# Kernel optimization log

Measured on AMD Instinct MI355X. Metric: run time of the kernel, lower is better.

Reference implementation:

```python
import jax, jax.numpy as jnp
import numpy as np

DEPTH = 10
LEAF = 2 ** DEPTH          # 1024 leaves
NODE_NUM = 2 * LEAF - 1    # 2047
N = NODE_NUM + 1           # 2048 nodes incl. global node 0
ATTN = 4
D = 128
B = 8
L = 2


def _trace_children(ni):
    terms = []
    s, e = ni << 1, (ni << 1) | 1
    while s <= NODE_NUM and e <= NODE_NUM:
        terms.extend(range(s, e + 1))
        s <<= 1
        e = (e << 1) | 1
    return terms


def _trace_left(si):
    ni, cd, terms, stop = si + LEAF, DEPTH, [], False
    while not stop:
        cs = ni - ATTN + 1 - ((ni - ATTN + 1) & 1)
        stop = cs < 2 ** cd
        cs = max(2 ** cd, cs)
        terms.extend(range(cs, ni + 1))
        ni = (cs - 1) >> 1
        cd -= 1
    return terms


def _trace_right(ei):
    ni, cd, terms, stop = ei + LEAF, DEPTH, [], False
    while not stop:
        ce = ni + ATTN - 1 + ((ni - ATTN) & 1)
        stop = ce >= 2 ** (cd + 1)
        ce = min(2 ** (cd + 1) - 1, ce)
        terms.extend(range(ni, ce + 1))
        ni = (ce + 1) >> 1
        cd -= 1
    return terms


def _build_edges():
    src, dst = [], []
    for ni in range(1, NODE_NUM + 1):
        if ni < LEAF:
            t = _trace_children(ni)
        else:
            t = _trace_left(ni - LEAF) + _trace_right(ni - LEAF)
        src.extend(t)
        dst.extend([ni] * len(t))
    e = np.stack([np.asarray(src, np.int64), np.asarray(dst, np.int64)])  # [2, E]
    off = np.arange(B, dtype=np.int64) * N
    eb = (e[:, None, :] + off[None, :, None]).reshape(2, -1)  # batch-offset like _fetch_edge_data
    return eb.astype(np.int32)


def setup_inputs() -> dict:
    key = jax.random.key(0)
    k0, k1, k2 = jax.random.split(key, 3)
    s = 1.0 / np.sqrt(D)
    return {
        "elements": jax.random.normal(k0, (B, LEAF, D), jnp.float32),
        "ln_gamma": jnp.ones((L, D), jnp.float32),
        "ln_beta": jnp.zeros((L, D), jnp.float32),
        "w_nei": (jax.random.normal(k1, (L, D, D), jnp.float32) * s),
        "b_nei": jnp.zeros((L, D), jnp.float32),
        "w_root": (jax.random.normal(k2, (L, D, D), jnp.float32) * s),
        "edge_index": jnp.asarray(_build_edges()),
    }


def _sinusoid(pos, d):
    # ArbitraryPositionEncoder: sinusoidal encoding over (possibly negative) positions
    half = d // 2
    inv = jnp.exp(-jnp.arange(half, dtype=jnp.float32) * (np.log(10000.0) / half))
    ang = pos[:, None] * inv[None, :]  # [n, half]
    return jnp.stack([jnp.sin(ang), jnp.cos(ang)], -1).reshape(pos.shape[0], d)


def reference(elements, ln_gamma, ln_beta, w_nei, b_nei, w_root, edge_index):
    Bx, leaf, d = elements.shape
    depth = int(np.log2(leaf))
    # bottom-up tree compression (mean of two children)
    cur = elements
    levels = [cur]
    for _ in range(depth):
        cur = 0.5 * (cur[:, 0::2] + cur[:, 1::2])
        levels.append(cur)
    # node ordering: [global node 0 (=-1), root (level 0), ..., leaves (level depth)]
    node_feat = jnp.concatenate(
        [jnp.full((Bx, 1, d), -1.0, elements.dtype)] + levels[::-1], axis=1)  # [B, N, D]
    n = node_feat.shape[1]
    # positional encoding: vertical = floor(log2(idx)), horizontal = idx - 2^vertical
    idx = jnp.arange(n, dtype=jnp.float32)
    vpos = jnp.floor(jnp.log2(jnp.where(idx == 0, 0.5, idx)))
    hpos = idx - jnp.exp2(vpos)
    enc = jnp.concatenate([_sinusoid(hpos, d // 2), _sinusoid(vpos, d // 2)], -1)  # [N, D]
    x = (node_feat + enc[None]).reshape(Bx * n, d)
    src, dst = edge_index[0], edge_index[1]
    nseg = Bx * n
    deg = jnp.maximum(
        jax.ops.segment_sum(jnp.ones(src.shape, jnp.float32), dst, num_segments=nseg), 1.0)
    # DeepGCNLayer res+ blocks with SAGEConv (mean aggr)
    for l in range(ln_gamma.shape[0]):
        mu = jnp.mean(x, -1, keepdims=True)
        var = jnp.mean((x - mu) ** 2, -1, keepdims=True)
        h = (x - mu) * jax.lax.rsqrt(var + 1e-5) * ln_gamma[l] + ln_beta[l]
        h = jax.nn.gelu(h, approximate=False)
        agg = jax.ops.segment_sum(h[src], dst, num_segments=nseg) / deg[:, None]
        h = agg @ w_nei[l] + b_nei[l] + h @ w_root[l]
        x = x + h
    return x.reshape(Bx, n, d)
```

## Files before the change

### kernel.cpp

```cpp
#include <hip/hip_runtime.h>
#include <hip/hip_bf16.h>

#define LEAFN 1024
#define NN    2048
#define BATCH 8
#define DD    128
#define ROWS  (BATCH*NN)
#define AHS   384
#define NB    256
#define NT    1024

#define LOG1E4_OVER_32 0.28782313662425575f

#define SLACK 9
#define CSTRIDE 136
#define SB_OFF   0
#define SBT      520
#define MSK_OFF  58240
#define DEG_OFF  59264
#define FB_OFF   59392
#define AGGL_OFF 0
#define RED_OFF  61440
#define RED2_OFF 62464

typedef __bf16 bf16x8 __attribute__((ext_vector_type(8)));
typedef float  floatx4 __attribute__((ext_vector_type(4)));
typedef float  floatx2 __attribute__((ext_vector_type(2)));

__device__ __forceinline__ float bf2f(unsigned short u) {
  return __uint_as_float(((unsigned)u) << 16);
}
__device__ __forceinline__ unsigned short f2bf(float f) {
  unsigned u = __float_as_uint(f);
  u += 0x7FFFu + ((u >> 16) & 1u);
  return (unsigned short)(u >> 16);
}
__device__ __forceinline__ float gelu(float v) {
  return 0.5f * v * (1.0f + erff(v * 0.70710678118f));
}
__device__ __forceinline__ floatx2 bfpair(unsigned u) {
  floatx2 r;
  r[0] = __uint_as_float(u << 16);
  r[1] = __uint_as_float(u & 0xffff0000u);
  return r;
}

__device__ __forceinline__ float enc_val(int node, int d) {
  float hp, vp;
  if (node == 0) { hp = -0.5f; vp = -1.0f; }
  else {
    int v = 31 - __clz(node);
    hp = (float)(node - (1 << v));
    vp = (float)v;
  }
  float pos = (d < 64) ? hp : vp;
  int i = ((d < 64) ? d : (d - 64)) >> 1;
  float inv = __expf(-(float)i * LOG1E4_OVER_32);
  float ang = pos * inv;
  return (d & 1) ? __cosf(ang) : __sinf(ang);
}

__device__ __forceinline__ void win_cd(int jb, int cd, int& lo_, int& wd_) {
  int g0 = 1024 + jb * 32, g1 = g0 + 31;
  int a0 = g0 >> (10 - cd), a1 = g1 >> (10 - cd);
  int l = a0 - SLACK, h = a1 + SLACK;
  int lvlo = 1 << cd, lvhi = (2 << cd) - 1;
  lo_ = l < lvlo ? lvlo : l;
  int hh = h > lvhi ? lvhi : h;
  int w = hh - lo_ + 1;
  wd_ = w < 0 ? 0 : w;
}

__device__ __forceinline__ void gbarN(int* bar, int slot) {
  __syncthreads();
  if (threadIdx.x == 0) {
    int g = blockIdx.x & 7;
    int* base = bar + (slot * 8 + g) * 64;
    __threadfence();
    if (__hip_atomic_fetch_add(base, 1, __ATOMIC_RELAXED,
                               __HIP_MEMORY_SCOPE_AGENT) == 31)
      __hip_atomic_store(base + 32, 1, __ATOMIC_RELAXED,
                         __HIP_MEMORY_SCOPE_AGENT);
    while (!__hip_atomic_load(base + 32, __ATOMIC_RELAXED,
                              __HIP_MEMORY_SCOPE_AGENT))
      __builtin_amdgcn_s_sleep(1);
    __threadfence();
  }
  __syncthreads();
}

__device__ __forceinline__ void st_agg(unsigned short* ah, int b, int g, int j,
                                       floatx4 S, float inv) {
  ushort4 o;
  o.x = f2bf(S[0] * inv); o.y = f2bf(S[1] * inv);
  o.z = f2bf(S[2] * inv); o.w = f2bf(S[3] * inv);
  *(ushort4*)&ah[(size_t)(b * NN + g) * AHS + j * 4] = o;
}

__device__ __forceinline__ void ph_tree(char* smemc, int b, int s,
                                        const float* __restrict__ elements,
                                        float* __restrict__ x,
                                        float* __restrict__ lvl4,
                                        unsigned short* __restrict__ ah,
                                        const float* __restrict__ gamma,
                                        const float* __restrict__ beta,
                                        float* __restrict__ sroot,
                                        float* xci, int* bar) {
  float* sm = (float*)smemc;
  floatx4* smv = (floatx4*)smemc;
  int tid = threadIdx.x;
  const float4* src = (const float4*)(elements + (size_t)(b * LEAFN + s * 64) * DD);
  for (int i = tid; i < 2048; i += NT) {
    int f = i * 4;
    int j = f >> 7, d = f & 127;
    *(float4*)&sm[(63 + j) * DD + d] = src[i];
  }
  __syncthreads();
  {
    for (int idx = tid; idx < 16 * 32; idx += NT) {
      int k = 16 + (idx >> 5), j = idx & 31;
      floatx4 a = 0.5f * (smv[(4 * k - 1) * 32 + j] + smv[(4 * k) * 32 + j]);
      floatx4 c = 0.5f * (smv[(4 * k + 1) * 32 + j] + smv[(4 * k + 2) * 32 + j]);
      smv[(2 * k - 1) * 32 + j] = a;
      smv[(2 * k) * 32 + j] = c;
      smv[(k - 1) * 32 + j] = 0.5f * (a + c);
    }
    __syncthreads();
    for (int idx = tid; idx < 4 * 32; idx += NT) {
      int k = 4 + (idx >> 5), j = idx & 31;
      floatx4 a = 0.5f * (smv[(4 * k - 1) * 32 + j] + smv[(4 * k) * 32 + j]);
      floatx4 c = 0.5f * (smv[(4 * k + 1) * 32 + j] + smv[(4 * k + 2) * 32 + j]);
      smv[(2 * k - 1) * 32 + j] = a;
      smv[(2 * k) * 32 + j] = c;
      smv[(k - 1) * 32 + j] = 0.5f * (a + c);
    }
    __syncthreads();
    for (int idx = tid; idx < 32; idx += NT) {
      int j = idx;
      floatx4 a = 0.5f * (smv[3 * 32 + j] + smv[4 * 32 + j]);
      floatx4 c = 0.5f * (smv[5 * 32 + j] + smv[6 * 32 + j]);
      smv[1 * 32 + j] = a;
      smv[2 * 32 + j] = c;
      floatx4 r = 0.5f * (a + c);
      smv[j] = r;
      ((floatx4*)&lvl4[(size_t)(b * 16 + s) * DD])[j] = r;
    }
  }
  __syncthreads();
  if (tid == 0) {
    __threadfence();
    __hip_atomic_store(bar + 1536 + b * 64 + s * 4, 1, __ATOMIC_RELAXED,
                       __HIP_MEMORY_SCOPE_AGENT);
  }
  {
    int d2 = tid & 63;
    int i = d2 & 31;
    float inv = __expf(-(float)i * LOG1E4_OVER_32);
    bool lowhalf = d2 < 32;
    for (int idx2 = tid; idx2 < 127 * 64; idx2 += NT) {
      int row = idx2 >> 6;
      int k = row + 1;
      int lv = 31 - __clz(k);
      int g = ((16 + s) << lv) | (k - (1 << lv));
      float vp = (float)(lv + 4);
      float hp = (float)(g - (16 << lv));
      float pos = lowhalf ? hp : vp;
      float sv, cv;
      __sincosf(pos * inv, &sv, &cv);
      int base = row * DD + 2 * d2;
      float xv0 = sm[base] + sv;
      float xv1 = sm[base + 1] + cv;
      sm[base] = xv0; sm[base + 1] = xv1;
      if (k >= 64 || k <= 32) {
        float2 o = make_float2(xv0, xv1);
        *(float2*)&x[((size_t)(b * NN + g)) * DD + 2 * d2] = o;
      }
    }
  }
  __syncthreads();
// ... 61 lines not shown
      floatx4 sk = (smv[(2 * k - 1) * 32 + j] + smv[(2 * k) * 32 + j]) + (sa + sc);
      smv[(4 * k - 1) * 32 + j] = sa;
      smv[(4 * k + 1) * 32 + j] = sc;
      smv[(2 * k - 1) * 32 + j] = sk;
      st_agg(ah, b, ((16 + s) << 5) | (2 * k - 32), j, sa, 0.5f);
      st_agg(ah, b, ((16 + s) << 5) | (2 * k + 1 - 32), j, sc, 0.5f);
      st_agg(ah, b, ((16 + s) << 4) | (k - 16), j, sk, 1.0f / 6.0f);
    }
    __syncthreads();
    for (int idx = tid; idx < 4 * 32; idx += NT) {
      int k = 4 + (idx >> 5), j = idx & 31;
      floatx4 sa = (smv[(4 * k - 1) * 32 + j] + smv[(4 * k) * 32 + j]) +
                   (smv[(8 * k - 1) * 32 + j] + smv[(8 * k + 1) * 32 + j]);
      floatx4 sc = (smv[(4 * k + 1) * 32 + j] + smv[(4 * k + 2) * 32 + j]) +
                   (smv[(8 * k + 3) * 32 + j] + smv[(8 * k + 5) * 32 + j]);
      floatx4 sk = (smv[(2 * k - 1) * 32 + j] + smv[(2 * k) * 32 + j]) + (sa + sc);
      smv[(4 * k - 1) * 32 + j] = sa;
      smv[(4 * k + 1) * 32 + j] = sc;
      smv[(2 * k - 1) * 32 + j] = sk;
      st_agg(ah, b, ((16 + s) << 3) | (2 * k - 8), j, sa, 1.0f / 14.0f);
      st_agg(ah, b, ((16 + s) << 3) | (2 * k + 1 - 8), j, sc, 1.0f / 14.0f);
      st_agg(ah, b, ((16 + s) << 2) | (k - 4), j, sk, 1.0f / 30.0f);
    }
    __syncthreads();
    for (int idx = tid; idx < 32; idx += NT) {
      int j = idx;
      floatx4 sa = (smv[3 * 32 + j] + smv[4 * 32 + j]) +
                   (smv[7 * 32 + j] + smv[9 * 32 + j]);
      floatx4 sc = (smv[5 * 32 + j] + smv[6 * 32 + j]) +
                   (smv[11 * 32 + j] + smv[13 * 32 + j]);
      floatx4 sk = (smv[1 * 32 + j] + smv[2 * 32 + j]) + (sa + sc);
      st_agg(ah, b, ((16 + s) << 1) | 0, j, sa, 1.0f / 62.0f);
      st_agg(ah, b, ((16 + s) << 1) | 1, j, sc, 1.0f / 62.0f);
      st_agg(ah, b, (16 + s), j, sk, 1.0f / 126.0f);
      ((floatx4*)&sroot[(size_t)(b * 16 + s) * DD])[j] = sk;
    }
  }
}

__device__ __forceinline__ void ph_top(char* smemc, int b,
                                       const float* __restrict__ lvl4,
                                       unsigned short* __restrict__ ah,
                                       const float* __restrict__ gamma,
                                       const float* __restrict__ beta) {
  float (*xs)[DD] = (float(*)[DD])smemc;
  int tid = threadIdx.x;
  if (tid < 128) {
    int d = tid;
    float v[16];
    for (int j = 0; j < 16; ++j) v[j] = lvl4[(b * 16 + j) * DD + d];
    for (int j = 0; j < 8; ++j) v[j] = 0.5f * (v[2 * j] + v[2 * j + 1]);
    for (int j = 0; j < 8; ++j) xs[8 + j][d] = v[j] + enc_val(8 + j, d);
    for (int j = 0; j < 4; ++j) v[j] = 0.5f * (v[2 * j] + v[2 * j + 1]);
    for (int j = 0; j < 4; ++j) xs[4 + j][d] = v[j] + enc_val(4 + j, d);
    for (int j = 0; j < 2; ++j) v[j] = 0.5f * (v[2 * j] + v[2 * j + 1]);
    for (int j = 0; j < 2; ++j) xs[2 + j][d] = v[j] + enc_val(2 + j, d);
    v[0] = 0.5f * (v[0] + v[1]);
    xs[1][d] = v[0] + enc_val(1, d);
    xs[0][d] = -1.0f + enc_val(0, d);
  }
  __syncthreads();
  if (tid < 128) {
    int rr = tid >> 3, sub = tid & 7, dp = sub * 16;
    float w[16], s1 = 0.f, s2 = 0.f;
#pragma unroll
    for (int j = 0; j < 16; ++j) { w[j] = xs[rr][dp + j]; s1 += w[j]; s2 += w[j] * w[j]; }
    s1 += __shfl_xor(s1, 1); s2 += __shfl_xor(s2, 1);
    s1 += __shfl_xor(s1, 2); s2 += __shfl_xor(s2, 2);
    s1 += __shfl_xor(s1, 4); s2 += __shfl_xor(s2, 4);
    float mu = s1 * (1.0f / 128.0f);
    float var = s2 * (1.0f / 128.0f) - mu * mu;
    float rinv = rsqrtf(var + 1e-5f);
    __attribute__((aligned(16))) unsigned short o[16];
#pragma unroll
    for (int j = 0; j < 16; ++j)
      o[j] = f2bf(gelu((w[j] - mu) * rinv * gamma[dp + j] + beta[dp + j]));
    unsigned short* dst = &ah[(size_t)(b * NN + rr) * AHS + 128 + dp];
    *(uint4*)&dst[0] = *(uint4*)&o[0];
    *(uint4*)&dst[8] = *(uint4*)&o[8];
  }
  __syncthreads();
}

__device__ __forceinline__ void ph_aggsub(char* smemc, int b, int s,
                                          unsigned short* ah,
                                          float* __restrict__ sroot) {
  floatx4 (*S)[32] = (floatx4(*)[32])smemc;
  int tid = threadIdx.x;
  for (int idx = tid; idx < 32 * 32; idx += NT) {
    int k = 32 + (idx >> 5), q = idx & 31;
    int c = (16 + s) * 64 + (2 * k - 64);
    size_t a0 = (size_t)(b * NN + c) * AHS + 256 + q * 4;
    ushort4 u0 = *(const ushort4*)&ah[a0];
    ushort4 u1 = *(const ushort4*)&ah[a0 + AHS];
    floatx4 v;
    v[0] = bf2f(u0.x) + bf2f(u1.x);
    v[1] = bf2f(u0.y) + bf2f(u1.y);
    v[2] = bf2f(u0.z) + bf2f(u1.z);
    v[3] = bf2f(u0.w) + bf2f(u1.w);
    S[k][q] = v;
    st_agg(ah, b, (16 + s) * 32 + (k - 32), q, v, 0.5f);
  }
  __syncthreads();
  for (int idx = tid; idx < 8 * 32; idx += NT) {
    int k = 8 + (idx >> 5), q = idx & 31;
    size_t aa = (size_t)(b * NN + (((16 + s) << 5) | (4 * k - 32))) * AHS + 256 + q * 4;
    ushort4 u0 = *(const ushort4*)&ah[aa];
    ushort4 u1 = *(const ushort4*)&ah[aa + AHS];
    size_t ab = (size_t)(b * NN + (((16 + s) << 5) | (4 * k + 2 - 32))) * AHS + 256 + q * 4;
    ushort4 w0 = *(const ushort4*)&ah[ab];
    ushort4 w1 = *(const ushort4*)&ah[ab + AHS];
    size_t ac = (size_t)(b * NN + (((16 + s) << 4) | (2 * k - 16))) * AHS + 256 + q * 4;
    ushort4 h0 = *(const ushort4*)&ah[ac];
    ushort4 h1 = *(const ushort4*)&ah[ac + AHS];
    floatx4 s4a, s4b, s3;
    floatx4 sc0 = S[4 * k][q], sc1 = S[4 * k + 1][q];
    floatx4 sd0 = S[4 * k + 2][q], sd1 = S[4 * k + 3][q];
    s4a[0] = bf2f(u0.x) + bf2f(u1.x) + sc0[0] + sc1[0];
    s4a[1] = bf2f(u0.y) + bf2f(u1.y) + sc0[1] + sc1[1];
    s4a[2] = bf2f(u0.z) + bf2f(u1.z) + sc0[2] + sc1[2];
    s4a[3] = bf2f(u0.w) + bf2f(u1.w) + sc0[3] + sc1[3];
    s4b[0] = bf2f(w0.x) + bf2f(w1.x) + sd0[0] + sd1[0];
    s4b[1] = bf2f(w0.y) + bf2f(w1.y) + sd0[1] + sd1[1];
    s4b[2] = bf2f(w0.z) + bf2f(w1.z) + sd0[2] + sd1[2];
    s4b[3] = bf2f(w0.w) + bf2f(w1.w) + sd0[3] + sd1[3];
    s3[0] = bf2f(h0.x) + bf2f(h1.x) + s4a[0] + s4b[0];
    s3[1] = bf2f(h0.y) + bf2f(h1.y) + s4a[1] + s4b[1];
    s3[2] = bf2f(h0.z) + bf2f(h1.z) + s4a[2] + s4b[2];
    s3[3] = bf2f(h0.w) + bf2f(h1.w) + s4a[3] + s4b[3];
    S[2 * k][q] = s4a; S[2 * k + 1][q] = s4b; S[k][q] = s3;
    st_agg(ah, b, ((16 + s) << 4) | (2 * k - 16), q, s4a, 1.0f / 6.0f);
    st_agg(ah, b, ((16 + s) << 4) | (2 * k + 1 - 16), q, s4b, 1.0f / 6.0f);
    st_agg(ah, b, ((16 + s) << 3) | (k - 8), q, s3, 1.0f / 14.0f);
  }
  __syncthreads();
  for (int idx = tid; idx < 2 * 32; idx += NT) {
    int k = 2 + (idx >> 5), q = idx & 31;
    size_t aa = (size_t)(b * NN + (((16 + s) << 3) | (4 * k - 8))) * AHS + 256 + q * 4;
    ushort4 u0 = *(const ushort4*)&ah[aa];
    ushort4 u1 = *(const ushort4*)&ah[aa + AHS];
    size_t ab = (size_t)(b * NN + (((16 + s) << 3) | (4 * k + 2 - 8))) * AHS + 256 + q * 4;
    ushort4 w0 = *(const ushort4*)&ah[ab];
    ushort4 w1 = *(const ushort4*)&ah[ab + AHS];
    size_t ac = (size_t)(b * NN + (((16 + s) << 2) | (2 * k - 4))) * AHS + 256 + q * 4;
    ushort4 h0 = *(const ushort4*)&ah[ac];
    ushort4 h1 = *(const ushort4*)&ah[ac + AHS];
    floatx4 s2a, s2b, s1v;
    floatx4 sc0 = S[4 * k][q], sc1 = S[4 * k + 1][q];
    floatx4 sd0 = S[4 * k + 2][q], sd1 = S[4 * k + 3][q];
    s2a[0] = bf2f(u0.x) + bf2f(u1.x) + sc0[0] + sc1[0];
    s2a[1] = bf2f(u0.y) + bf2f(u1.y) + sc0[1] + sc1[1];
    s2a[2] = bf2f(u0.z) + bf2f(u1.z) + sc0[2] + sc1[2];
    s2a[3] = bf2f(u0.w) + bf2f(u1.w) + sc0[3] + sc1[3];
    s2b[0] = bf2f(w0.x) + bf2f(w1.x) + sd0[0] + sd1[0];
    s2b[1] = bf2f(w0.y) + bf2f(w1.y) + sd0[1] + sd1[1];
    s2b[2] = bf2f(w0.z) + bf2f(w1.z) + sd0[2] + sd1[2];
    s2b[3] = bf2f(w0.w) + bf2f(w1.w) + sd0[3] + sd1[3];
    s1v[0] = bf2f(h0.x) + bf2f(h1.x) + s2a[0] + s2b[0];
    s1v[1] = bf2f(h0.y) + bf2f(h1.y) + s2a[1] + s2b[1];
    s1v[2] = bf2f(h0.z) + bf2f(h1.z) + s2a[2] + s2b[2];
    s1v[3] = bf2f(h0.w) + bf2f(h1.w) + s2a[3] + s2b[3];
    S[2 * k][q] = s2a; S[2 * k + 1][q] = s2b; S[k][q] = s1v;
    st_agg(ah, b, ((16 + s) << 2) | (2 * k - 4), q, s2a, 1.0f / 30.0f);
    st_agg(ah, b, ((16 + s) << 2) | (2 * k + 1 - 4), q, s2b, 1.0f / 30.0f);
    st_agg(ah, b, ((16 + s) << 1) | (k - 2), q, s1v, 1.0f / 62.0f);
  }
  __syncthreads();
  for (int idx = tid; idx < 32; idx += NT) {
    int q = idx;
    size_t aa = (size_t)(b * NN + (((16 + s) << 1) | 0)) * AHS + 256 + q * 4;
    ushort4 u0 = *(const ushort4*)&ah[aa];
    ushort4 u1 = *(const ushort4*)&ah[aa + AHS];
    floatx4 sc0 = S[2][q], sc1 = S[3][q];
    floatx4 s0v;
    s0v[0] = bf2f(u0.x) + bf2f(u1.x) + sc0[0] + sc1[0];
    s0v[1] = bf2f(u0.y) + bf2f(u1.y) + sc0[1] + sc1[1];
    s0v[2] = bf2f(u0.z) + bf2f(u1.z) + sc0[2] + sc1[2];
    s0v[3] = bf2f(u0.w) + bf2f(u1.w) + sc0[3] + sc1[3];
    st_agg(ah, b, (16 + s), q, s0v, 1.0f / 126.0f);
    ((floatx4*)sroot)[(size_t)(b * 16 + s) * 32 + q] = s0v;
  }
}

__device__ __forceinline__ void ph_leafagg(char* smemc, int b, int jb,
                                           const int* __restrict__ srcv,
                                           const int* __restrict__ dstv,
                                           const int* __restrict__ s0a,
                                           const int* __restrict__ s1a,
                                           const unsigned short* __restrict__ eoff,
                                           unsigned short* ah, int hoff,
                                           int build) {
  int tid = threadIdx.x;
  int lane = tid & 63, wv = tid >> 6;
  unsigned short* SB = (unsigned short*)(smemc + SB_OFF);
  unsigned* msk = (unsigned*)(smemc + MSK_OFF);
  float* invdeg = (float*)(smemc + DEG_OFF);
  unsigned int* fb = (unsigned int*)(smemc + FB_OFF);
  unsigned short* aggl = (unsigned short*)(smemc + AGGL_OFF);
  int rbase = b * NN + 1024 + jb * 32;

  int lo[11], wd[11], off[11];
  int acc_off = 0;
#pragma unroll
  for (int cd = 10; cd >= 1; --cd) {
    win_cd(jb, cd, lo[cd], wd[cd]);
    off[cd] = acc_off;
    acc_off += wd[cd];
  }

  for (int t = tid; t < 3640; t += NT)
    ((uint4*)smemc)[t] = make_uint4(0, 0, 0, 0);
  if (build) {
    if (tid < 256) msk[tid] = 0u;
    if (tid >= 256 && tid < 288)
      invdeg[tid - 256] = 1.0f /
          (float)max(s1a[rbase + tid - 256] - s0a[rbase + tid - 256], 1);
    if (tid == 288) *fb = 0u;
  }
  __syncthreads();

  if (build) {
    int E0 = s0a[rbase], E1 = s1a[rbase + 31];
    for (int e = E0 + tid; e < E1; e += NT) {
      int leaf = dstv[e] - rbase;
      unsigned kr = eoff[e];
      if (kr == 0xFFFFu) atomicOr(fb, 1u << leaf);
      else atomicOr(&msk[leaf * 8 + (kr >> 5)], 1u << (kr & 31));
    }
  }
#pragma unroll
  for (int cd = 10; cd >= 1; --cd) {
    int w = wd[cd];
    for (int t = tid; t < w * 16; t += NT) {
      int row = t >> 4, seg = t & 15;
      int kr = off[cd] + row;
      uint4 u = *(const uint4*)&ah[(size_t)(b * NN + lo[cd] + row) * AHS + hoff + seg * 8];
      unsigned short* p = SB + ((kr >> 5) * 8 + (seg >> 1)) * SBT +
                          ((kr & 31) >> 3) * 128 + (seg & 1) * 64 + (kr & 7);
      p[0]  = (unsigned short)(u.x & 0xffff);
      p[8]  = (unsigned short)(u.x >> 16);
      p[16] = (unsigned short)(u.y & 0xffff);
      p[24] = (unsigned short)(u.y >> 16);
      p[32] = (unsigned short)(u.z & 0xffff);
      p[40] = (unsigned short)(u.z >> 16);
      p[48] = (unsigned short)(u.w & 0xffff);
      p[56] = (unsigned short)(u.w >> 16);
    }
  }
  __syncthreads();

  int m = lane & 15, q = lane >> 4;
  int mt = wv >> 3, nt = wv & 7;
  int arow = mt * 16 + m;
  floatx4 acc = (floatx4){0.f, 0.f, 0.f, 0.f};
#pragma unroll
  for (int kcl = 0; kcl < 7; ++kcl) {
    unsigned mw = msk[arow * 8 + kcl];
    unsigned bits = (mw >> (q * 8)) & 0xffu;
    union { uint4 u; bf16x8 v; } A;
    A.u.x = ((bits & 1u)  ? 0x3F80u : 0u) | ((bits & 2u)   ? 0x3F800000u : 0u);
    A.u.y = ((bits & 4u)  ? 0x3F80u : 0u) | ((bits & 8u)   ? 0x3F800000u : 0u);
    A.u.z = ((bits & 16u) ? 0x3F80u : 0u) | ((bits & 32u)  ? 0x3F800000u : 0u);
    A.u.w = ((bits & 64u) ? 0x3F80u : 0u) | ((bits & 128u) ? 0x3F800000u : 0u);
    bf16x8 bb = *(const bf16x8*)&SB[(kcl * 8 + nt) * SBT + lane * 8];
    acc = __builtin_amdgcn_mfma_f32_16x16x32_bf16(A.v, bb, acc, 0, 0, 0);
  }
  __syncthreads();

  unsigned fbm = *fb;
#pragma unroll
  for (int r = 0; r < 4; ++r) {
    int leaf = mt * 16 + q * 4 + r;
    if (!((fbm >> leaf) & 1u))
      aggl[leaf * CSTRIDE + nt * 16 + m] = f2bf(acc[r] * invdeg[leaf]);
  }
  if (fbm && tid < 512) {
    int leaf = tid >> 4, c = tid & 15;
    if ((fbm >> leaf) & 1u) {
      int e0 = s0a[rbase + leaf], e1 = s1a[rbase + leaf];
      floatx2 a0 = {0.f, 0.f}, a1 = {0.f, 0.f}, a2 = {0.f, 0.f}, a3 = {0.f, 0.f};
      for (int e = e0; e < e1; ++e) {
        int g = srcv[e] - b * NN;
        uint4 u = *(const uint4*)&ah[(size_t)(b * NN + g) * AHS + hoff + c * 8];
        a0 += bfpair(u.x); a1 += bfpair(u.y); a2 += bfpair(u.z); a3 += bfpair(u.w);
      }
      float inv = 1.0f / (float)max(e1 - e0, 1);
      __attribute__((aligned(16))) unsigned short o[8];
      o[0] = f2bf(a0[0] * inv); o[1] = f2bf(a0[1] * inv);
      o[2] = f2bf(a1[0] * inv); o[3] = f2bf(a1[1] * inv);
      o[4] = f2bf(a2[0] * inv); o[5] = f2bf(a2[1] * inv);
      o[6] = f2bf(a3[0] * inv); o[7] = f2bf(a3[1] * inv);
      *(uint4*)&aggl[leaf * CSTRIDE + c * 8] = *(uint4*)&o[0];
    }
  }
}

__device__ __forceinline__ void ph_topfin(int b,
                                          const float* __restrict__ sroot,
                                          unsigned short* ah, int hoff) {
  int d = threadIdx.x;
  float S16[16], h16[16], Sv[16];
#pragma unroll
  for (int j = 0; j < 16; ++j) S16[j] = sroot[(size_t)(b * 16 + j) * DD + d];
#pragma unroll
  for (int j = 0; j < 16; ++j)
    h16[j] = bf2f(ah[(size_t)(b * NN + 16 + j) * AHS + hoff + d]);
#pragma unroll
  for (int k = 8; k < 16; ++k)
    Sv[k] = h16[2 * k - 16] + h16[2 * k - 15] + S16[2 * k - 16] + S16[2 * k - 15];
#pragma unroll
  for (int k = 7; k >= 1; --k)
    Sv[k] = bf2f(ah[(size_t)(b * NN + 2 * k) * AHS + hoff + d]) +
            bf2f(ah[(size_t)(b * NN + 2 * k + 1) * AHS + hoff + d]) +
            Sv[2 * k] + Sv[2 * k + 1];
#pragma unroll
  for (int k = 1; k < 16; ++k) {
    int dv = 31 - __clz(k);
    float inv = 1.0f / (float)((1 << (11 - dv)) - 2);
    ah[(size_t)(b * NN + k) * AHS + d] = f2bf(Sv[k] * inv);
  }
  ah[(size_t)(b * NN) * AHS + d] = f2bf(0.0f);
}

__device__ __forceinline__ void ph_gemm32(char* redc, const unsigned short* aggl,
                                          int rowbase, unsigned short* ah,
                                          const unsigned short* __restrict__ wfl,
                                          const float* __restrict__ bn,
                                          float* __restrict__ x, int hoff_in,
                                          const float* __restrict__ gamma,
                                          const float* __restrict__ beta,
                                          float* xc, int first_layer) {
  int wave = threadIdx.x >> 6, lane = threadIdx.x & 63;
  bool act = wave < 8;
  int wl = wave & 7;
  int mt = wl >> 2, nq = wl & 3;
  int r0 = rowbase + mt * 16;
  int m = lane & 15, q = lane >> 4;
  floatx4 acc[2];
  acc[0] = (floatx4){0.f, 0.f, 0.f, 0.f};
  acc[1] = (floatx4){0.f, 0.f, 0.f, 0.f};
  if (act) {
    const unsigned short* arow = ah + (size_t)(r0 + m) * AHS + q * 8;
    const bf16x8* B = (const bf16x8*)wfl + lane;
#pragma unroll
    for (int kc = 0; kc < 8; ++kc) {
      bf16x8 a0;
      if (kc < 4)
        a0 = *(const bf16x8*)&aggl[(mt * 16 + m) * CSTRIDE + kc * 32 + q * 8];
      else
        a0 = *(const bf16x8*)(arow + hoff_in + (kc - 4) * 32);
#pragma unroll
      for (int ci = 0; ci < 2; ++ci) {
        bf16x8 bb = B[(kc * 8 + nq * 2 + ci) * 64];
        acc[ci] = __builtin_amdgcn_mfma_f32_16x16x32_bf16(a0, bb, acc[ci], 0, 0, 0);
      }
    }
  }
  if (first_layer) {
    float s1[4] = {0.f, 0.f, 0.f, 0.f}, s2[4] = {0.f, 0.f, 0.f, 0.f};
    if (act) {
#pragma unroll
      for (int ci = 0; ci < 2; ++ci) {
        int col = (nq * 2 + ci) * 16 + m;
        float bias = bn[col];
#pragma unroll
        for (int r = 0; r < 4; ++r) {
          int row = r0 + q * 4 + r;
          float v = x[(size_t)row * DD + col] + acc[ci][r] + bias;
          xc[ci * 4 + r] = v;
          s1[r] += v; s2[r] += v * v;
        }
      }
#pragma unroll
      for (int r = 0; r < 4; ++r) {
        s1[r] += __shfl_xor(s1[r], 1); s2[r] += __shfl_xor(s2[r], 1);
// ... 181 lines not shown
  floatx4 acc = (floatx4){0.f, 0.f, 0.f, 0.f};
  int col = (ct & 7) * 16 + m;
  if (act) {
    const unsigned short* arow = ah + (size_t)(b * NN + m) * AHS + q * 8;
    const bf16x8* B = (const bf16x8*)wfl + lane;
#pragma unroll
    for (int kc = 0; kc < 8; ++kc) {
      int koff = (kc < 4) ? kc * 32 : hoff_in + (kc - 4) * 32;
      bf16x8 a0 = *(const bf16x8*)(arow + koff);
      bf16x8 bb = B[(kc * 8 + ct) * 64];
      acc = __builtin_amdgcn_mfma_f32_16x16x32_bf16(a0, bb, acc, 0, 0, 0);
    }
  }
  if (first_layer) {
    float s1[4] = {0.f, 0.f, 0.f, 0.f}, s2[4] = {0.f, 0.f, 0.f, 0.f};
    float bias = act ? bn[col] : 0.f;
    if (act) {
#pragma unroll
      for (int r = 0; r < 4; ++r) {
        float v = xc[r] + acc[r] + bias;
        xc[r] = v; s1[r] = v; s2[r] = v * v;
      }
#pragma unroll
      for (int r = 0; r < 4; ++r) {
        s1[r] += __shfl_xor(s1[r], 1); s2[r] += __shfl_xor(s2[r], 1);
        s1[r] += __shfl_xor(s1[r], 2); s2[r] += __shfl_xor(s2[r], 2);
        s1[r] += __shfl_xor(s1[r], 4); s2[r] += __shfl_xor(s2[r], 4);
        s1[r] += __shfl_xor(s1[r], 8); s2[r] += __shfl_xor(s2[r], 8);
      }
    }
    float* red = (float*)redc;
    __syncthreads();
    if (act && m == 0) {
#pragma unroll
      for (int r = 0; r < 4; ++r) {
        red[(q * 4 + r) * 8 + ct] = s1[r];
        red[128 + (q * 4 + r) * 8 + ct] = s2[r];
      }
    }
    __syncthreads();
    if (act) {
#pragma unroll
      for (int r = 0; r < 4; ++r) {
        float t1 = 0.f, t2 = 0.f;
#pragma unroll
        for (int j = 0; j < 8; ++j) {
          t1 += red[(q * 4 + r) * 8 + j];
          t2 += red[128 + (q * 4 + r) * 8 + j];
        }
        float mu = t1 * (1.0f / 128.0f);
        float var = t2 * (1.0f / 128.0f) - mu * mu;
        float rv = rsqrtf(var + 1e-5f);
        float hh = gelu((xc[r] - mu) * rv * gamma[col] + beta[col]);
        ah[(size_t)(b * NN + q * 4 + r) * AHS + 256 + col] = f2bf(hh);
      }
    }
  } else {
    if (act) {
      float bias = bn[col];
#pragma unroll
      for (int r = 0; r < 4; ++r)
        x[(size_t)(b * NN + q * 4 + r) * DD + col] = xc[r] + acc[r] + bias;
    }
  }
}

__global__ __launch_bounds__(NT, 1) void k_mega(
    const float* __restrict__ elements, const float* __restrict__ ln_gamma,
    const float* __restrict__ ln_beta, const float* __restrict__ w_nei,
    const float* __restrict__ b_nei, const float* __restrict__ w_root,
    const int* __restrict__ srcv, const int* __restrict__ dstv, int E,
    float* __restrict__ x, int* s0a, int* s1a, float* lvl4, float* sroot,
    unsigned short* wf, unsigned short* ah, unsigned short* eoff, int* bar) {
  __shared__ __align__(16) char smem[65536];
  int bid = blockIdx.x, tid = threadIdx.x;
  int b = bid & 7, gb = bid >> 3;
  int Eb = E >> 3;
  unsigned short* wfg = wf + (size_t)b * 65536;
  float xcl[8], xci[8], xct[4];
  int wv = tid >> 6;

  if (gb < 16) {
    ph_tree(smem, b, gb, elements, x, lvl4, ah, ln_gamma, ln_beta, sroot, xci, bar);
  } else if (gb < 24) {
    int base = b * Eb;
    for (int i = base + (gb - 16) * NT + tid; i < base + Eb; i += 8 * NT) {
      int dv = dstv[i];
      if (i == 0 || dstv[i - 1] != dv) s0a[dv] = i;
      if (i == base + Eb - 1 || dstv[i + 1] != dv) s1a[dv] = i + 1;
    }
    for (int i = base + (gb - 16) * NT + tid; i < base + Eb; i += 8 * NT) {
      int dl = dstv[i] - b * NN - 1024;
      unsigned short ov = 0xFFFFu;
      if (dl >= 0) {
        int jb2 = dl >> 5;
        int g = srcv[i] - b * NN;
        int lv = 31 - __clz(g);
        int acc2 = 0;
#pragma unroll
        for (int cd = 10; cd >= 1; --cd) {
          int lo_, wd_;
          win_cd(jb2, cd, lo_, wd_);
          if (cd == lv) {
            int idx = g - lo_;
            if ((unsigned)idx < (unsigned)wd_)
              ov = (unsigned short)(acc2 + idx);
          }
          acc2 += wd_;
        }
      }
      eoff[i] = ov;
    }
  } else if (gb < 28) {
    int gi = (gb - 24) * NT + tid;
    int lane = gi & 63, ct = (gi >> 6) & 7, kc = gi >> 9;
    int n = ct * 16 + (lane & 15);
    int k = kc * 32 + (lane >> 4) * 8;
    int kk = k & 127;
#pragma unroll
    for (int l = 0; l < 2; ++l) {
      const float* w = (k < 128) ? (w_nei + (size_t)l * DD * DD)
                                 : (w_root + (size_t)l * DD * DD);
      unsigned short* o = wfg + (size_t)l * 32768 + (size_t)gi * 8;
#pragma unroll
      for (int j = 0; j < 8; ++j) o[j] = f2bf(w[(size_t)(kk + j) * DD + n]);
    }
  } else if (gb == 28) {
    if (tid < 16) {
      while (!__hip_atomic_load(bar + 1536 + b * 64 + tid * 4, __ATOMIC_RELAXED,
                                __HIP_MEMORY_SCOPE_AGENT))
        __builtin_amdgcn_s_sleep(1);
      __threadfence();
    }
    __syncthreads();
    ph_top(smem, b, lvl4, ah, ln_gamma, ln_beta);
    {
      int ln = tid & 63, m_ = ln & 15, q_ = ln >> 4;
      if (wv < 8) {
        float (*xs)[DD] = (float(*)[DD])smem;
#pragma unroll
        for (int r = 0; r < 4; ++r) xct[r] = xs[q_ * 4 + r][wv * 16 + m_];
      }
    }
  }
  gbarN(bar, 0);

  if (gb == 28) {
    if (tid < 128) ph_topfin(b, sroot, ah, 128);
    __syncthreads();
    ph_gemm16t(smem + RED_OFF, b, ah, wfg, b_nei, x, 128,
               ln_gamma + DD, ln_beta + DD, xct, 1);
    __syncthreads();
  }
  ph_leafagg(smem, b, gb, srcv, dstv, s0a, s1a, eoff, ah, 128, 1);
  __syncthreads();
  if (wv < 8) {
    ph_gemm32(smem + RED_OFF, (const unsigned short*)(smem + AGGL_OFF),
              b * NN + 1024 + gb * 32, ah, wfg, b_nei, x, 128,
              ln_gamma + DD, ln_beta + DD, xcl, 1);
  } else if (gb < 16) {
    ph_gemm32s(smem + RED2_OFF, b, gb, 32, ah, wfg, b_nei, x, 128,
               ln_gamma + DD, ln_beta + DD, xci, 1, nullptr);
  } else {
    ph_gemm32s(smem + RED2_OFF, b, gb - 16, 0, ah, wfg, b_nei, x, 128,
               ln_gamma + DD, ln_beta + DD, xci, 1, x);
  }
  gbarN(bar, 1);

  if (gb < 16) {
    ph_aggsub(smem, b, gb, ah, sroot);
    __syncthreads();
    if (tid == 0) {
      __threadfence();
      __hip_atomic_store(bar + 1024 + b * 64 + gb * 4, 1, __ATOMIC_RELAXED,
                         __HIP_MEMORY_SCOPE_AGENT);
    }
  }
  ph_leafagg(smem, b, gb, srcv, dstv, s0a, s1a, eoff, ah, 256, 0);
  if (gb >= 16 && tid == 0) {
    while (!__hip_atomic_load(bar + 1024 + b * 64 + (gb - 16) * 4, __ATOMIC_RELAXED,
                              __HIP_MEMORY_SCOPE_AGENT))
      __builtin_amdgcn_s_sleep(1);
    __threadfence();
  }
  __syncthreads();
  if (wv < 8) {
    ph_gemm32(smem + RED_OFF, (const unsigned short*)(smem + AGGL_OFF),
              b * NN + 1024 + gb * 32, ah, wfg + 32768, b_nei + DD,
              x, 256, ln_gamma, ln_beta, xcl, 0);
  } else if (gb < 16) {
    ph_gemm32s(smem + RED2_OFF, b, gb, 32, ah, wfg + 32768, b_nei + DD, x, 256,
               ln_gamma, ln_beta, xci, 0, nullptr);
  } else {
    ph_gemm32s(smem + RED2_OFF, b, gb - 16, 0, ah, wfg + 32768, b_nei + DD, x, 256,
               ln_gamma, ln_beta, xci, 0, nullptr);
  }
  if (gb == 28) {
    if (tid < 16) {
      while (!__hip_atomic_load(bar + 1024 + b * 64 + tid * 4, __ATOMIC_RELAXED,
                                __HIP_MEMORY_SCOPE_AGENT))
        __builtin_amdgcn_s_sleep(1);
      __threadfence();
    }
    __syncthreads();
    if (tid < 128) ph_topfin(b, sroot, ah, 256);
    __syncthreads();
    ph_gemm16t(smem + RED_OFF, b, ah, wfg + 32768, b_nei + DD, x, 256,
               ln_gamma, ln_beta, xct, 0);
  }
}

extern "C" void kernel_launch(void* const* d_in, const int* in_sizes, int n_in,
                              void* d_out, int out_size, void* d_ws, size_t ws_size,
                              hipStream_t stream) {
  const float* elements = (const float*)d_in[0];
  const float* ln_gamma = (const float*)d_in[1];
  const float* ln_beta  = (const float*)d_in[2];
  const float* w_nei    = (const float*)d_in[3];
  const float* b_nei    = (const float*)d_in[4];
  const float* w_root   = (const float*)d_in[5];
  const int*   edge     = (const int*)d_in[6];
  int E = in_sizes[6] / 2;
  const int* srcv = edge;
  const int* dstv = edge + E;
  float* x = (float*)d_out;

  char* ws = (char*)d_ws;
  int*            bar   = (int*)ws;
  int*            s0    = (int*)(ws + 65536);
  int*            s1    = (int*)(ws + 131072);
  float*          lvl4  = (float*)(ws + 196608);
  float*          sroot = (float*)(ws + 262144);
  unsigned short* wf    = (unsigned short*)(ws + 327680);
  unsigned short* ah    = (unsigned short*)(ws + 327680 + 1048576);
  unsigned short* eoff  = (unsigned short*)(ws + 327680 + 1048576 + 12582912);

  hipMemsetAsync(bar, 0, 8192, stream);
  k_mega<<<dim3(NB), dim3(NT), 0, stream>>>(
      elements, ln_gamma, ln_beta, w_nei, b_nei, w_root,
      srcv, dstv, E, x, s0, s1, lvl4, sroot, wf, ah, eoff, bar);
}
```

Baseline: 158.1 us.

## Overlap subtree aggregation with leaf aggregation using warp specialization

Folds the separate subtree aggregation phase into the leaf aggregation routine. Waves 14-15 (threads 896+) run the per-column subtree sums from registers while the other waves stage the neighbour tile and run the MFMA mask-matmul. The MFMA now uses 8 waves, each doing two 16-row tiles. The shared-memory zeroing is narrowed to the tail rows, and the mask clearing is moved before the global barrier. This removes several block-wide syncs and serial phases, but puts a 64-float register array on the specialist threads, which may raise register pressure.

```diff
diff --git a/kernel.cpp b/kernel.cpp
--- a/kernel.cpp
+++ b/kernel.cpp
@@ -95,6 +95,65 @@
   o.x = f2bf(S[0] * inv); o.y = f2bf(S[1] * inv);
   o.z = f2bf(S[2] * inv); o.w = f2bf(S[3] * inv);
   *(ushort4*)&ah[(size_t)(b * NN + g) * AHS + j * 4] = o;
+}
+
+__device__ __forceinline__ void aggsub_A(int b, int s, unsigned short* ah,
+                                         float* S, int d) {
+#pragma unroll
+  for (int k = 32; k < 64; ++k) {
+    int c = ((16 + s) << 6) | (2 * k - 64);
+    size_t a = (size_t)(b * NN + c) * AHS + 256 + d;
+    float v = bf2f(ah[a]) + bf2f(ah[a + AHS]);
+    S[k] = v;
+    ah[(size_t)(b * NN + (((16 + s) << 5) | (k - 32))) * AHS + d] = f2bf(v * 0.5f);
+  }
+#pragma unroll
+  for (int k = 16; k < 32; ++k) {
+    int c = ((16 + s) << 5) | (2 * k - 32);
+    size_t a = (size_t)(b * NN + c) * AHS + 256 + d;
+    float v = bf2f(ah[a]) + bf2f(ah[a + AHS]) + S[2 * k] + S[2 * k + 1];
+    S[k] = v;
+    ah[(size_t)(b * NN + (((16 + s) << 4) | (k - 16))) * AHS + d] =
+        f2bf(v * (1.0f / 6.0f));
+  }
+}
+__device__ __forceinline__ void aggsub_B(int b, int s, unsigned short* ah,
+                                         float* __restrict__ sroot,
+                                         float* S, int d) {
+#pragma unroll
+  for (int k = 8; k < 16; ++k) {
+    int c = ((16 + s) << 4) | (2 * k - 16);
+    size_t a = (size_t)(b * NN + c) * AHS + 256 + d;
+    float v = bf2f(ah[a]) + bf2f(ah[a + AHS]) + S[2 * k] + S[2 * k + 1];
+    S[k] = v;
+    ah[(size_t)(b * NN + (((16 + s) << 3) | (k - 8))) * AHS + d] =
+        f2bf(v * (1.0f / 14.0f));
+  }
+#pragma unroll
+  for (int k = 4; k < 8; ++k) {
+    int c = ((16 + s) << 3) | (2 * k - 8);
+    size_t a = (size_t)(b * NN + c) * AHS + 256 + d;
+    float v = bf2f(ah[a]) + bf2f(ah[a + AHS]) + S[2 * k] + S[2 * k + 1];
+    S[k] = v;
+    ah[(size_t)(b * NN + (((16 + s) << 2) | (k - 4))) * AHS + d] =
+        f2bf(v * (1.0f / 30.0f));
+  }
+#pragma unroll
+  for (int k = 2; k < 4; ++k) {
+    int c = ((16 + s) << 2) | (2 * k - 4);
+    size_t a = (size_t)(b * NN + c) * AHS + 256 + d;
+    float v = bf2f(ah[a]) + bf2f(ah[a + AHS]) + S[2 * k] + S[2 * k + 1];
+    S[k] = v;
+    ah[(size_t)(b * NN + (((16 + s) << 1) | (k - 2))) * AHS + d] =
+        f2bf(v * (1.0f / 62.0f));
+  }
+  {
+    int c = (16 + s) << 1;
+    size_t a = (size_t)(b * NN + c) * AHS + 256 + d;
+    float v = bf2f(ah[a]) + bf2f(ah[a + AHS]) + S[2] + S[3];
+    ah[(size_t)(b * NN + (16 + s)) * AHS + d] = f2bf(v * (1.0f / 126.0f));
+    sroot[(size_t)(b * 16 + s) * DD + d] = v;
+  }
 }
 
 __device__ __forceinline__ void ph_tree(char* smemc, int b, int s,
@@ -322,106 +381,6 @@
   __syncthreads();
 }
 
-__device__ __forceinline__ void ph_aggsub(char* smemc, int b, int s,
-                                          unsigned short* ah,
-                                          float* __restrict__ sroot) {
-  floatx4 (*S)[32] = (floatx4(*)[32])smemc;
-  int tid = threadIdx.x;
-  for (int idx = tid; idx < 32 * 32; idx += NT) {
-    int k = 32 + (idx >> 5), q = idx & 31;
-    int c = (16 + s) * 64 + (2 * k - 64);
-    size_t a0 = (size_t)(b * NN + c) * AHS + 256 + q * 4;
-    ushort4 u0 = *(const ushort4*)&ah[a0];
-    ushort4 u1 = *(const ushort4*)&ah[a0 + AHS];
-    floatx4 v;
-    v[0] = bf2f(u0.x) + bf2f(u1.x);
-    v[1] = bf2f(u0.y) + bf2f(u1.y);
-    v[2] = bf2f(u0.z) + bf2f(u1.z);
-    v[3] = bf2f(u0.w) + bf2f(u1.w);
-    S[k][q] = v;
-    st_agg(ah, b, (16 + s) * 32 + (k - 32), q, v, 0.5f);
-  }
-  __syncthreads();
-  for (int idx = tid; idx < 8 * 32; idx += NT) {
-    int k = 8 + (idx >> 5), q = idx & 31;
-    size_t aa = (size_t)(b * NN + (((16 + s) << 5) | (4 * k - 32))) * AHS + 256 + q * 4;
-    ushort4 u0 = *(const ushort4*)&ah[aa];
-    ushort4 u1 = *(const ushort4*)&ah[aa + AHS];
-    size_t ab = (size_t)(b * NN + (((16 + s) << 5) | (4 * k + 2 - 32))) * AHS + 256 + q * 4;
-    ushort4 w0 = *(const ushort4*)&ah[ab];
-    ushort4 w1 = *(const ushort4*)&ah[ab + AHS];
-    size_t ac = (size_t)(b * NN + (((16 + s) << 4) | (2 * k - 16))) * AHS + 256 + q * 4;
-    ushort4 h0 = *(const ushort4*)&ah[ac];
-    ushort4 h1 = *(const ushort4*)&ah[ac + AHS];
-    floatx4 s4a, s4b, s3;
-    floatx4 sc0 = S[4 * k][q], sc1 = S[4 * k + 1][q];
-    floatx4 sd0 = S[4 * k + 2][q], sd1 = S[4 * k + 3][q];
-    s4a[0] = bf2f(u0.x) + bf2f(u1.x) + sc0[0] + sc1[0];
-    s4a[1] = bf2f(u0.y) + bf2f(u1.y) + sc0[1] + sc1[1];
-    s4a[2] = bf2f(u0.z) + bf2f(u1.z) + sc0[2] + sc1[2];
-    s4a[3] = bf2f(u0.w) + bf2f(u1.w) + sc0[3] + sc1[3];
-    s4b[0] = bf2f(w0.x) + bf2f(w1.x) + sd0[0] + sd1[0];
-    s4b[1] = bf2f(w0.y) + bf2f(w1.y) + sd0[1] + sd1[1];
-    s4b[2] = bf2f(w0.z) + bf2f(w1.z) + sd0[2] + sd1[2];
-    s4b[3] = bf2f(w0.w) + bf2f(w1.w) + sd0[3] + sd1[3];
-    s3[0] = bf2f(h0.x) + bf2f(h1.x) + s4a[0] + s4b[0];
-    s3[1] = bf2f(h0.y) + bf2f(h1.y) + s4a[1] + s4b[1];
-    s3[2] = bf2f(h0.z) + bf2f(h1.z) + s4a[2] + s4b[2];
-    s3[3] = bf2f(h0.w) + bf2f(h1.w) + s4a[3] + s4b[3];
-    S[2 * k][q] = s4a; S[2 * k + 1][q] = s4b; S[k][q] = s3;
-    st_agg(ah, b, ((16 + s) << 4) | (2 * k - 16), q, s4a, 1.0f / 6.0f);
-    st_agg(ah, b, ((16 + s) << 4) | (2 * k + 1 - 16), q, s4b, 1.0f / 6.0f);
-    st_agg(ah, b, ((16 + s) << 3) | (k - 8), q, s3, 1.0f / 14.0f);
-  }
-  __syncthreads();
-  for (int idx = tid; idx < 2 * 32; idx += NT) {
-    int k = 2 + (idx >> 5), q = idx & 31;
-    size_t aa = (size_t)(b * NN + (((16 + s) << 3) | (4 * k - 8))) * AHS + 256 + q * 4;
-    ushort4 u0 = *(const ushort4*)&ah[aa];
-    ushort4 u1 = *(const ushort4*)&ah[aa + AHS];
-    size_t ab = (size_t)(b * NN + (((16 + s) << 3) | (4 * k + 2 - 8))) * AHS + 256 + q * 4;
-    ushort4 w0 = *(const ushort4*)&ah[ab];
-    ushort4 w1 = *(const ushort4*)&ah[ab + AHS];
-    size_t ac = (size_t)(b * NN + (((16 + s) << 2) | (2 * k - 4))) * AHS + 256 + q * 4;
-    ushort4 h0 = *(const ushort4*)&ah[ac];
-    ushort4 h1 = *(const ushort4*)&ah[ac + AHS];
-    floatx4 s2a, s2b, s1v;
-    floatx4 sc0 = S[4 * k][q], sc1 = S[4 * k + 1][q];
-    floatx4 sd0 = S[4 * k + 2][q], sd1 = S[4 * k + 3][q];
-    s2a[0] = bf2f(u0.x) + bf2f(u1.x) + sc0[0] + sc1[0];
-    s2a[1] = bf2f(u0.y) + bf2f(u1.y) + sc0[1] + sc1[1];
-    s2a[2] = bf2f(u0.z) + bf2f(u1.z) + sc0[2] + sc1[2];
-    s2a[3] = bf2f(u0.w) + bf2f(u1.w) + sc0[3] + sc1[3];
-    s2b[0] = bf2f(w0.x) + bf2f(w1.x) + sd0[0] + sd1[0];
-    s2b[1] = bf2f(w0.y) + bf2f(w1.y) + sd0[1] + sd1[1];
-    s2b[2] = bf2f(w0.z) + bf2f(w1.z) + sd0[2] + sd1[2];
-    s2b[3] = bf2f(w0.w) + bf2f(w1.w) + sd0[3] + sd1[3];
-    s1v[0] = bf2f(h0.x) + bf2f(h1.x) + s2a[0] + s2b[0];
-    s1v[1] = bf2f(h0.y) + bf2f(h1.y) + s2a[1] + s2b[1];
-    s1v[2] = bf2f(h0.z) + bf2f(h1.z) + s2a[2] + s2b[2];
-    s1v[3] = bf2f(h0.w) + bf2f(h1.w) + s2a[3] + s2b[3];
-    S[2 * k][q] = s2a; S[2 * k + 1][q] = s2b; S[k][q] = s1v;
-    st_agg(ah, b, ((16 + s) << 2) | (2 * k - 4), q, s2a, 1.0f / 30.0f);
-    st_agg(ah, b, ((16 + s) << 2) | (2 * k + 1 - 4), q, s2b, 1.0f / 30.0f);
-    st_agg(ah, b, ((16 + s) << 1) | (k - 2), q, s1v, 1.0f / 62.0f);
-  }
-  __syncthreads();
-  for (int idx = tid; idx < 32; idx += NT) {
-    int q = idx;
-    size_t aa = (size_t)(b * NN + (((16 + s) << 1) | 0)) * AHS + 256 + q * 4;
-    ushort4 u0 = *(const ushort4*)&ah[aa];
-    ushort4 u1 = *(const ushort4*)&ah[aa + AHS];
-    floatx4 sc0 = S[2][q], sc1 = S[3][q];
-    floatx4 s0v;
-    s0v[0] = bf2f(u0.x) + bf2f(u1.x) + sc0[0] + sc1[0];
-    s0v[1] = bf2f(u0.y) + bf2f(u1.y) + sc0[1] + sc1[1];
-    s0v[2] = bf2f(u0.z) + bf2f(u1.z) + sc0[2] + sc1[2];
-    s0v[3] = bf2f(u0.w) + bf2f(u1.w) + sc0[3] + sc1[3];
-    st_agg(ah, b, (16 + s), q, s0v, 1.0f / 126.0f);
-    ((floatx4*)sroot)[(size_t)(b * 16 + s) * 32 + q] = s0v;
-  }
-}
-
 __device__ __forceinline__ void ph_leafagg(char* smemc, int b, int jb,
                                            const int* __restrict__ srcv,
                                            const int* __restrict__ dstv,
@@ -429,7 +388,8 @@
                                            const int* __restrict__ s1a,
                                            const unsigned short* __restrict__ eoff,
                                            unsigned short* ah, int hoff,
-                                           int build) {
+                                           int build, int do_agg,
+                                           float* __restrict__ sroot) {
   int tid = threadIdx.x;
   int lane = tid & 63, wv = tid >> 6;
   unsigned short* SB = (unsigned short*)(smemc + SB_OFF);
@@ -448,89 +408,110 @@
     acc_off += wd[cd];
   }
 
-  for (int t = tid; t < 3640; t += NT)
-    ((uint4*)smemc)[t] = make_uint4(0, 0, 0, 0);
-  if (build) {
-    if (tid < 256) msk[tid] = 0u;
-    if (tid >= 256 && tid < 288)
-      invdeg[tid - 256] = 1.0f /
-          (float)max(s1a[rbase + tid - 256] - s0a[rbase + tid - 256], 1);
-    if (tid == 288) *fb = 0u;
-  }
-  __syncthreads();
-
-  if (build) {
-    int E0 = s0a[rbase], E1 = s1a[rbase + 31];
-    for (int e = E0 + tid; e < E1; e += NT) {
-      int leaf = dstv[e] - rbase;
-      unsigned kr = eoff[e];
-      if (kr == 0xFFFFu) atomicOr(fb, 1u << leaf);
-      else atomicOr(&msk[leaf * 8 + (kr >> 5)], 1u << (kr & 31));
-    }
-  }
-#pragma unroll
-  for (int cd = 10; cd >= 1; --cd) {
-    int w = wd[cd];
-    for (int t = tid; t < w * 16; t += NT) {
-      int row = t >> 4, seg = t & 15;
-      int kr = off[cd] + row;
-      uint4 u = *(const uint4*)&ah[(size_t)(b * NN + lo[cd] + row) * AHS + hoff + seg * 8];
+  float S[64];
+
+  if (tid < 896) {
+    if (build) {
+      int E0 = s0a[rbase], E1 = s1a[rbase + 31];
+      for (int e = E0 + tid; e < E1; e += 896) {
+        int leaf = dstv[e] - rbase;
+        unsigned kr = eoff[e];
+        if (kr == 0xFFFFu) atomicOr(fb, 1u << leaf);
+        else atomicOr(&msk[leaf * 8 + (kr >> 5)], 1u << (kr & 31));
+      }
+      if (tid < 32)
+        invdeg[tid] = 1.0f / (float)max(s1a[rbase + tid] - s0a[rbase + tid], 1);
+    }
+#pragma unroll
+    for (int cd = 10; cd >= 1; --cd) {
+      int w = wd[cd];
+      for (int t = tid; t < w * 16; t += 896) {
+        int row = t >> 4, seg = t & 15;
+        int kr = off[cd] + row;
+        uint4 u = *(const uint4*)&ah[(size_t)(b * NN + lo[cd] + row) * AHS + hoff + seg * 8];
+        unsigned short* p = SB + ((kr >> 5) * 8 + (seg >> 1)) * SBT +
+                            ((kr & 31) >> 3) * 128 + (seg & 1) * 64 + (kr & 7);
+        p[0]  = (unsigned short)(u.x & 0xffff);
+        p[8]  = (unsigned short)(u.x >> 16);
+        p[16] = (unsigned short)(u.y & 0xffff);
+        p[24] = (unsigned short)(u.y >> 16);
+        p[32] = (unsigned short)(u.z & 0xffff);
+        p[40] = (unsigned short)(u.z >> 16);
+        p[48] = (unsigned short)(u.w & 0xffff);
+        p[56] = (unsigned short)(u.w >> 16);
+      }
+    }
+    int ntail = (224 - acc_off) * 16;
+    for (int t = tid; t < ntail; t += 896) {
+      int kr = acc_off + (t >> 4), seg = t & 15;
       unsigned short* p = SB + ((kr >> 5) * 8 + (seg >> 1)) * SBT +
                           ((kr & 31) >> 3) * 128 + (seg & 1) * 64 + (kr & 7);
-      p[0]  = (unsigned short)(u.x & 0xffff);
-      p[8]  = (unsigned short)(u.x >> 16);
-      p[16] = (unsigned short)(u.y & 0xffff);
-      p[24] = (unsigned short)(u.y >> 16);
-      p[32] = (unsigned short)(u.z & 0xffff);
-      p[40] = (unsigned short)(u.z >> 16);
-      p[48] = (unsigned short)(u.w & 0xffff);
-      p[56] = (unsigned short)(u.w >> 16);
-    }
+      p[0] = 0; p[8] = 0; p[16] = 0; p[24] = 0;
+      p[32] = 0; p[40] = 0; p[48] = 0; p[56] = 0;
+    }
+  } else if (do_agg) {
+    aggsub_A(b, jb, ah, S, tid - 896);
   }
   __syncthreads();
 
   int m = lane & 15, q = lane >> 4;
-  int mt = wv >> 3, nt = wv & 7;
-  int arow = mt * 16 + m;
-  floatx4 acc = (floatx4){0.f, 0.f, 0.f, 0.f};
-#pragma unroll
-  for (int kcl = 0; kcl < 7; ++kcl) {
-    unsigned mw = msk[arow * 8 + kcl];
-    unsigned bits = (mw >> (q * 8)) & 0xffu;
-    union { uint4 u; bf16x8 v; } A;
-    A.u.x = ((bits & 1u)  ? 0x3F80u : 0u) | ((bits & 2u)   ? 0x3F800000u : 0u);
-    A.u.y = ((bits & 4u)  ? 0x3F80u : 0u) | ((bits & 8u)   ? 0x3F800000u : 0u);
-    A.u.z = ((bits & 16u) ? 0x3F80u : 0u) | ((bits & 32u)  ? 0x3F800000u : 0u);
-    A.u.w = ((bits & 64u) ? 0x3F80u : 0u) | ((bits & 128u) ? 0x3F800000u : 0u);
-    bf16x8 bb = *(const bf16x8*)&SB[(kcl * 8 + nt) * SBT + lane * 8];
-    acc = __builtin_amdgcn_mfma_f32_16x16x32_bf16(A.v, bb, acc, 0, 0, 0);
-  }
-  __syncthreads();
-
-  unsigned fbm = *fb;
-#pragma unroll
-  for (int r = 0; r < 4; ++r) {
-    int leaf = mt * 16 + q * 4 + r;
-    if (!((fbm >> leaf) & 1u))
-      aggl[leaf * CSTRIDE + nt * 16 + m] = f2bf(acc[r] * invdeg[leaf]);
-  }
-  if (fbm && tid < 512) {
-    int leaf = tid >> 4, c = tid & 15;
-    if ((fbm >> leaf) & 1u) {
-      int e0 = s0a[rbase + leaf], e1 = s1a[rbase + leaf];
-      floatx2 a0 = {0.f, 0.f}, a1 = {0.f, 0.f}, a2 = {0.f, 0.f}, a3 = {0.f, 0.f};
-      for (int e = e0; e < e1; ++e) {
-        int g = srcv[e] - b * NN;
-        uint4 u = *(const uint4*)&ah[(size_t)(b * NN + g) * AHS + hoff + c * 8];
-        a0 += bfpair(u.x); a1 += bfpair(u.y); a2 += bfpair(u.z); a3 += bfpair(u.w);
-      }
-      float inv = 1.0f / (float)max(e1 - e0, 1);
-      __attribute__((aligned(16))) unsigned short o[8];
-      o[0] = f2bf(a0[0] * inv); o[1] = f2bf(a0[1] * inv);
-      o[2] = f2bf(a1[0] * inv); o[3] = f2bf(a1[1] * inv);
-      o[4] = f2bf(a2[0] * inv); o[5] = f2bf(a2[1] * inv);
-      o[6] = f2bf(a3[0] * inv); o[7] = f2bf(a3[1] * inv);
-      *(uint4*)&aggl[leaf * CSTRIDE + c * 8] = *(uint4*)&o[0];
+  floatx4 acc0 = (floatx4){0.f, 0.f, 0.f, 0.f};
+  floatx4 acc1 = (floatx4){0.f, 0.f, 0.f, 0.f};
+  if (wv < 8) {
+    int nt = wv;
+#pragma unroll
+    for (int kcl = 0; kcl < 7; ++kcl) {
+      bf16x8 bb = *(const bf16x8*)&SB[(kcl * 8 + nt) * SBT + lane * 8];
+      unsigned mw0 = msk[m * 8 + kcl];
+      unsigned mw1 = msk[(16 + m) * 8 + kcl];
+      unsigned b0 = (mw0 >> (q * 8)) & 0xffu;
+      unsigned b1 = (mw1 >> (q * 8)) & 0xffu;
+      union { uint4 u; bf16x8 v; } A0, A1;
+      A0.u.x = ((b0 & 1u)  ? 0x3F80u : 0u) | ((b0 & 2u)   ? 0x3F800000u : 0u);
+      A0.u.y = ((b0 & 4u)  ? 0x3F80u : 0u) | ((b0 & 8u)   ? 0x3F800000u : 0u);
+      A0.u.z = ((b0 & 16u) ? 0x3F80u : 0u) | ((b0 & 32u)  ? 0x3F800000u : 0u);
+      A0.u.w = ((b0 & 64u) ? 0x3F80u : 0u) | ((b0 & 128u) ? 0x3F800000u : 0u);
+      A1.u.x = ((b1 & 1u)  ? 0x3F80u : 0u) | ((b1 & 2u)   ? 0x3F800000u : 0u);
+      A1.u.y = ((b1 & 4u)  ? 0x3F80u : 0u) | ((b1 & 8u)   ? 0x3F800000u : 0u);
+      A1.u.z = ((b1 & 16u) ? 0x3F80u : 0u) | ((b1 & 32u)  ? 0x3F800000u : 0u);
+      A1.u.w = ((b1 & 64u) ? 0x3F80u : 0u) | ((b1 & 128u) ? 0x3F800000u : 0u);
+      acc0 = __builtin_amdgcn_mfma_f32_16x16x32_bf16(A0.v, bb, acc0, 0, 0, 0);
+      acc1 = __builtin_amdgcn_mfma_f32_16x16x32_bf16(A1.v, bb, acc1, 0, 0, 0);
+    }
+  } else if (do_agg && tid >= 896) {
+    aggsub_B(b, jb, ah, sroot, S, tid - 896);
+  }
+  __syncthreads();
+
+  if (wv < 8) {
+    unsigned fbm = *fb;
+    int nt = wv;
+#pragma unroll
+    for (int r = 0; r < 4; ++r) {
+      int l0 = q * 4 + r, l1 = 16 + q * 4 + r;
+      if (!((fbm >> l0) & 1u))
+        aggl[l0 * CSTRIDE + nt * 16 + m] = f2bf(acc0[r] * invdeg[l0]);
+      if (!((fbm >> l1) & 1u))
+        aggl[l1 * CSTRIDE + nt * 16 + m] = f2bf(acc1[r] * invdeg[l1]);
+    }
+    if (fbm && tid < 512) {
+      int leaf = tid >> 4, c = tid & 15;
+      if ((fbm >> leaf) & 1u) {
+        int e0 = s0a[rbase + leaf], e1 = s1a[rbase + leaf];
+        floatx2 a0 = {0.f, 0.f}, a1 = {0.f, 0.f}, a2 = {0.f, 0.f}, a3 = {0.f, 0.f};
+        for (int e = e0; e < e1; ++e) {
+          int g = srcv[e] - b * NN;
+          uint4 u = *(const uint4*)&ah[(size_t)(b * NN + g) * AHS + hoff + c * 8];
+          a0 += bfpair(u.x); a1 += bfpair(u.y); a2 += bfpair(u.z); a3 += bfpair(u.w);
+        }
+        float inv = 1.0f / (float)max(e1 - e0, 1);
+        __attribute__((aligned(16))) unsigned short o[8];
+        o[0] = f2bf(a0[0] * inv); o[1] = f2bf(a0[1] * inv);
+        o[2] = f2bf(a1[0] * inv); o[3] = f2bf(a1[1] * inv);
+        o[4] = f2bf(a2[0] * inv); o[5] = f2bf(a2[1] * inv);
+        o[6] = f2bf(a3[0] * inv); o[7] = f2bf(a3[1] * inv);
+        *(uint4*)&aggl[leaf * CSTRIDE + c * 8] = *(uint4*)&o[0];
+      }
     }
   }
 }
@@ -878,6 +859,7 @@
 
   if (gb < 16) {
     ph_tree(smem, b, gb, elements, x, lvl4, ah, ln_gamma, ln_beta, sroot, xci, bar);
+    __syncthreads();
   } else if (gb < 24) {
     int base = b * Eb;
     for (int i = base + (gb - 16) * NT + tid; i < base + Eb; i += 8 * NT) {
@@ -939,6 +921,7 @@
       }
     }
   }
+  if (tid < 289) *(unsigned*)(smem + MSK_OFF + 4 * tid) = 0u;
   gbarN(bar, 0);
 
   if (gb == 28) {
@@ -948,7 +931,7 @@
                ln_gamma + DD, ln_beta + DD, xct, 1);
     __syncthreads();
   }
-  ph_leafagg(smem, b, gb, srcv, dstv, s0a, s1a, eoff, ah, 128, 1);
+  ph_leafagg(smem, b, gb, srcv, dstv, s0a, s1a, eoff, ah, 128, 1, 0, sroot);
   __syncthreads();
   if (wv < 8) {
     ph_gemm32(smem + RED_OFF, (const unsigned short*)(smem + AGGL_OFF),
@@ -963,16 +946,13 @@
   }
   gbarN(bar, 1);
 
-  if (gb < 16) {
-    ph_aggsub(smem, b, gb, ah, sroot);
-    __syncthreads();
-    if (tid == 0) {
-      __threadfence();
-      __hip_atomic_store(bar + 1024 + b * 64 + gb * 4, 1, __ATOMIC_RELAXED,
-                         __HIP_MEMORY_SCOPE_AGENT);
-    }
-  }
-  ph_leafagg(smem, b, gb, srcv, dstv, s0a, s1a, eoff, ah, 256, 0);
+  ph_leafagg(smem, b, gb, srcv, dstv, s0a, s1a, eoff, ah, 256, 0,
+             (gb < 16) ? 1 : 0, sroot);
+  if (gb < 16 && tid == 0) {
+    __threadfence();
+    __hip_atomic_store(bar + 1024 + b * 64 + gb * 4, 1, __ATOMIC_RELAXED,
+                       __HIP_MEMORY_SCOPE_AGENT);
+  }
   if (gb >= 16 && tid == 0) {
     while (!__hip_atomic_load(bar + 1024 + b * 64 + (gb - 16) * 4, __ATOMIC_RELAXED,
                               __HIP_MEMORY_SCOPE_AGENT))
```

Result: no change. 160.1 us (+1.3%).
